# Performance work log

Measured on AMD Instinct MI355X. Metric: run time of the kernel, lower is better.

## Reference

```python
import jax, jax.numpy as jnp
import numpy as np

L = 512       # sequence length
N_AA = 21     # amino-acid alphabet size
D = 128       # per-residue substitution embedding dim
N1 = 256
N2 = 256


def setup_inputs() -> dict:
    key = jax.random.key(0)
    k1, k2, k3 = jax.random.split(key, 3)
    X1 = jax.random.randint(k1, (N1, L), 0, N_AA)
    X2 = jax.random.randint(k2, (N2, L), 0, N_AA)
    W = jax.random.normal(k3, (L * N_AA, N_AA * D), dtype=jnp.float32) * 0.02
    b = jnp.zeros((N_AA * D,), jnp.float32)
    w_param = jnp.zeros((L * (L - 1) // 2,), jnp.float32)
    a = jnp.ones((1,), jnp.float32)
    return {"X1": X1, "X2": X2, "W": W, "b": b, "w_param": w_param, "a": a}


def _network(X, W, b):
    # one-hot + linear stand-in for self.network; outputs (n, n_aa, d)
    n = X.shape[0]
    oh = jax.nn.one_hot(X, N_AA, dtype=W.dtype).reshape(n, -1)  # (n, L*n_aa)
    return (oh @ W + b).reshape(n, N_AA, -1)


def _wdk(subs, w):
    # torch: (subs[:, graph] * w).sum(2) * subs, summed over dim 1
    # graph[i] = arange(L), so this equals subs @ w^T contracted with subs:
    # out[..] = sum_i sum_j subs[.., i] * w[i, j] * subs[.., j]
    return jnp.einsum('...i,ij,...j->...', subs, w, subs)


def reference(X1, X2, W, b, w_param, a):
    n1, Lx = X1.shape
    n2 = X2.shape[0]

    # symmetric pairwise weight matrix; diagonal stays 0 -> sigmoid(0)=0.5
    i_x, i_y = np.tril_indices(Lx, k=-1)
    wm = jnp.zeros((Lx, Lx), W.dtype).at[i_x, i_y].set(w_param).at[i_y, i_x].set(w_param)
    w = jax.nn.sigmoid(wm)

    # per-sequence substitution matrices S = E E^T, (n, n_aa, n_aa)
    E1 = _network(X1, W, b)
    S1 = jnp.einsum('nad,nbd->nab', E1, E1)
    E2 = _network(X2, W, b)
    S2 = jnp.einsum('nad,nbd->nab', E2, E2)

    r1 = jnp.arange(n1)
    r2 = jnp.arange(n2)

    # self terms: subs[n, l] = S[n, X[n,l], X[n,l]]
    d1 = S1[r1[:, None], X1, X1]                  # (n1, L)
    k1 = _wdk(d1, w)[:, None]                     # (n1, 1)
    d2 = S2[r2[:, None], X2, X2]                  # (n2, L)
    k2 = _wdk(d2, w)[None, :]                     # (1, n2)

    # cross terms: average of the two sequences' S, gathered directly
    # (avoids materializing the (n1*n2, n_aa, n_aa) averaged S tensor)
    g1 = S1[r1[:, None, None], X1[:, None, :], X2[None, :, :]]  # (n1, n2, L)
    g2 = S2[r2[None, :, None], X1[:, None, :], X2[None, :, :]]  # (n1, n2, L)
    subs = 0.5 * (g1 + g2)

    K = _wdk(subs, w)                             # (n1, n2)
    K = K / jnp.sqrt(k1) / jnp.sqrt(k2)
    return (a ** 2) * K
```

## Files before the change

kernel.cpp:

```cpp
#include <hip/hip_runtime.h>
#include <cstdint>
#include <cstddef>

typedef __attribute__((ext_vector_type(8))) __bf16 bf16x8;
typedef __attribute__((ext_vector_type(4))) float f32x4;
typedef __attribute__((ext_vector_type(16))) float f32x16;

__device__ __forceinline__ unsigned short f2b(float x) {
    uint32_t u = __float_as_uint(x);
    u += 0x7FFFu + ((u >> 16) & 1u);
    return (unsigned short)(u >> 16);
}
__device__ __forceinline__ float b2f(unsigned short h) {
    return __uint_as_float(((uint32_t)h) << 16);
}

__device__ __forceinline__ void gl16(const unsigned short* g, unsigned short* l) {
    __builtin_amdgcn_global_load_lds((const __attribute__((address_space(1))) uint32_t*)g,
                                     (__attribute__((address_space(3))) uint32_t*)l, 16, 0, 0);
}

#define L_SEQ 512
#define N_AA 21
#define DDIM 128
#define NCOL 2688
#define NSEQ 512
#define TBSTRIDE 448
#define KTOT 10752
#define ZCH 12
#define KBTOT 672
#define KBCH 56

#define PB_WBZ   14112
#define PB_EINIT 5376
#define PB_REPACK 1024
#define PB_WBUILD 1024
#define PB_ABZ   2688
#define PB_TOTAL (PB_WBZ + PB_EINIT + PB_REPACK + PB_WBUILD + PB_ABZ)

__global__ __launch_bounds__(256) void prep_kernel(const int* X1, const int* X2,
                                                   const float* W, const float* bvec, const float* wp,
                                                   uint8_t* X8,
                                                   float* w32, unsigned short* wswz,
                                                   float* E, unsigned short* Wbz, unsigned short* Abz) {
    int bid = blockIdx.x;
    int t = threadIdx.x;
    if (bid < PB_WBZ) {
        int f = bid * 4 + (t >> 6);
        int lane = t & 63, lr = lane & 31, hf = lane >> 5;
        int cb = f / KBTOT, kb = f - cb * KBTOT;
        const float* src = W + (size_t)(kb * 16 + hf * 8) * NCOL + cb * 32 + lr;
        union { uint4 q; unsigned short s[8]; } o;
#pragma unroll
        for (int j = 0; j < 8; ++j) o.s[j] = f2b(src[(size_t)j * NCOL]);
        *(uint4*)&Wbz[(size_t)f * 512 + lane * 8] = o.q;
        return;
    }
    bid -= PB_WBZ;
    if (bid < PB_EINIT) {
        int e = bid * 256 + t;
        E[e] = bvec[e % NCOL];
        return;
    }
    bid -= PB_EINIT;
    if (bid < PB_REPACK) {
        int e = bid * 256 + t;
        if (e < 131072) X8[e] = (uint8_t)X1[e];
        else            X8[e] = (uint8_t)X2[e - 131072];
        return;
    }
    bid -= PB_REPACK;
    if (bid < PB_WBUILD) {
        int e = bid * 256 + t;
        int p = e >> 9, q = e & 511;
        float x = 0.0f;
        if (p > q)      x = wp[p * (p - 1) / 2 + q];
        else if (p < q) x = wp[q * (q - 1) / 2 + p];
        float s = 1.0f / (1.0f + expf(-x));
        w32[e] = s;
        int nb = p >> 5, lr = p & 31;
        int kb = q >> 4, hf = (q >> 3) & 1, j = q & 7;
        wswz[(size_t)((nb * 32 + kb) * 512) + (hf * 32 + lr) * 8 + j] = f2b(s);
        return;
    }
    bid -= PB_WBUILD;
    {
        int f = bid * 4 + (t >> 6);
        int lane = t & 63, lr = lane & 31, hf = lane >> 5;
        int mb = f / KBTOT, kb = f - mb * KBTOT;
        int m = mb * 32 + lr;
        const int* Xrow = (m < 256) ? (X1 + (size_t)m * L_SEQ) : (X2 + (size_t)(m - 256) * L_SEQ);
        int k0 = kb * 16 + hf * 8;
        union { uint4 q; unsigned short s[8]; } o;
#pragma unroll
        for (int j = 0; j < 8; ++j) {
            int k = k0 + j;
            int l = k / N_AA;
            int aa = k - l * N_AA;
            o.s[j] = (Xrow[l] == aa) ? (unsigned short)0x3F80u : (unsigned short)0u;
        }
        *(uint4*)&Abz[(size_t)f * 512 + lane * 8] = o.q;
    }
}

__global__ __launch_bounds__(256, 4) void e_mfma_v3(const unsigned short* Abz, const unsigned short* Wbz, float* E) {
    __shared__ unsigned short lds[4 * 8 * 512];

    int lin = blockIdx.x;
    int s = ((lin & 7) * 126) + (lin >> 3);
    int cx = s % 21;
    int rem = s / 21;
    int my = rem & 3;
    int kz = rem >> 2;

    int t = threadIdx.x, wid = t >> 6, lane = t & 63;
    int lr = lane & 31, hf = lane >> 5;
    int kb0 = kz * KBCH;

    const unsigned short* Aw = Abz + ((size_t)((my * 4 + wid) * KBTOT + kb0)) * 512 + lane * 8;
    const unsigned short* Bw = Wbz + ((size_t)((cx * 4 + wid) * KBTOT + kb0)) * 512 + lane * 8;
    unsigned short* La = &lds[wid * 512];
    unsigned short* Lb = &lds[(4 + wid) * 512];

#define STG(buf_, kb_) do { \
        gl16(Aw + (size_t)(kb_) * 512, La + (buf_) * 4096); \
        gl16(Bw + (size_t)(kb_) * 512, Lb + (buf_) * 4096); \
    } while (0)

    int alo = (wid & 1) * 2;
    int blo = 4 + (wid >> 1) * 2;

    f32x16 acc00, acc01, acc10, acc11;
#pragma unroll
    for (int r = 0; r < 16; ++r) { acc00[r] = 0.f; acc01[r] = 0.f; acc10[r] = 0.f; acc11[r] = 0.f; }

#define COMPUTE(kb_) do { \
        const unsigned short* base = &lds[((kb_) & 3) * 4096]; \
        bf16x8 a0 = *(const bf16x8*)(base + (alo + 0) * 512 + lane * 8); \
        bf16x8 a1 = *(const bf16x8*)(base + (alo + 1) * 512 + lane * 8); \
        bf16x8 b0 = *(const bf16x8*)(base + (blo + 0) * 512 + lane * 8); \
        bf16x8 b1 = *(const bf16x8*)(base + (blo + 1) * 512 + lane * 8); \
        acc00 = __builtin_amdgcn_mfma_f32_32x32x16_bf16(a0, b0, acc00, 0, 0, 0); \
        acc01 = __builtin_amdgcn_mfma_f32_32x32x16_bf16(a0, b1, acc01, 0, 0, 0); \
        acc10 = __builtin_amdgcn_mfma_f32_32x32x16_bf16(a1, b0, acc10, 0, 0, 0); \
        acc11 = __builtin_amdgcn_mfma_f32_32x32x16_bf16(a1, b1, acc11, 0, 0, 0); \
    } while (0)

    STG(0, 0); STG(1, 1); STG(2, 2);

#pragma unroll 1
    for (int kb = 0; kb < KBCH - 3; ++kb) {
        STG((kb + 3) & 3, kb + 3);
        asm volatile("s_waitcnt vmcnt(6)" ::: "memory");
        __builtin_amdgcn_s_barrier();
        __builtin_amdgcn_sched_barrier(0);
        COMPUTE(kb);
        __builtin_amdgcn_sched_barrier(0);
        __builtin_amdgcn_s_barrier();
    }
    asm volatile("s_waitcnt vmcnt(4)" ::: "memory");
    __builtin_amdgcn_s_barrier();
    __builtin_amdgcn_sched_barrier(0);
    COMPUTE(53);
    asm volatile("s_waitcnt vmcnt(2)" ::: "memory");
    __builtin_amdgcn_s_barrier();
    __builtin_amdgcn_sched_barrier(0);
    COMPUTE(54);
    asm volatile("s_waitcnt vmcnt(0)" ::: "memory");
    __builtin_amdgcn_s_barrier();
    __builtin_amdgcn_sched_barrier(0);
    COMPUTE(55);

#undef STG
#undef COMPUTE

    int mb0 = my * 4 + (wid & 1) * 2;
    int cb0 = cx * 4 + (wid >> 1) * 2;
#pragma unroll
    for (int r = 0; r < 16; ++r) {
        int row = (r & 3) + 8 * (r >> 2) + 4 * hf;
        float* base = E + (size_t)(mb0 * 32 + row) * NCOL + cb0 * 32 + lr;
        atomicAdd(base, acc00[r]);
        atomicAdd(base + 32, acc01[r]);
        atomicAdd(base + (size_t)32 * NCOL, acc10[r]);
        atomicAdd(base + (size_t)32 * NCOL + 32, acc11[r]);
    }
}

__global__ __launch_bounds__(256) void t_kernel(const float* E, unsigned short* Tb, float* Tdiag) {
    __shared__ float4 Es4[21 * 33];
    int t = threadIdx.x, n = blockIdx.x;
    for (int e = t; e < 21 * 32; e += 256) {
        int r = e >> 5, d = e & 31;
        Es4[r * 33 + d] = *(const float4*)(E + (size_t)n * NCOL + r * 128 + d * 4);
    }
    __syncthreads();
    for (int e = t; e < 441; e += 256) {
        int r = e / 21, c = e - r * 21;
        const float4* ar = &Es4[r * 33];
        const float4* br = &Es4[c * 33];
        float s = 0.f;
#pragma unroll 8
        for (int d = 0; d < 32; ++d) {
            float4 a = ar[d], b = br[d];
            s += a.x * b.x + a.y * b.y + a.z * b.z + a.w * b.w;
        }
        Tb[(size_t)n * TBSTRIDE + e] = f2b(0.5f * s);
        if (r == c) Tdiag[n * 24 + r] = s;
    }
}

__global__ __launch_bounds__(256) void k_kernel(const uint8_t* X8, const float* Tdiag, const float* w32, float* kinv) {
    __shared__ __align__(16) float dvec[4][512];
    __shared__ float Td[4][21];
    __shared__ float red[4][256];
    int t = threadIdx.x, n0 = blockIdx.x * 4;
    if (t < 84) Td[t / 21][t % 21] = Tdiag[(size_t)(n0 + t / 21) * 24 + (t % 21)];
    __syncthreads();
    for (int e = t; e < 2048; e += 256) {
        int nn = e >> 9, l = e & 511;
        dvec[nn][l] = Td[nn][X8[(size_t)(n0 + nn) * 512 + l]];
    }
    __syncthreads();
    float p0 = 0.f, p1 = 0.f, p2 = 0.f, p3 = 0.f;
    for (int p = t; p < 512; p += 256) {
        const float4* wr4 = (const float4*)(w32 + (size_t)p * 512);
        float d0 = 0.f, d1 = 0.f, d2 = 0.f, d3 = 0.f;
        for (int q = 0; q < 128; ++q) {
            float4 wv = wr4[q];
            float4 a = ((const float4*)dvec[0])[q];
            float4 b = ((const float4*)dvec[1])[q];
            float4 c = ((const float4*)dvec[2])[q];
            float4 d = ((const float4*)dvec[3])[q];
            d0 += wv.x * a.x + wv.y * a.y + wv.z * a.z + wv.w * a.w;
            d1 += wv.x * b.x + wv.y * b.y + wv.z * b.z + wv.w * b.w;
            d2 += wv.x * c.x + wv.y * c.y + wv.z * c.z + wv.w * c.w;
            d3 += wv.x * d.x + wv.y * d.y + wv.z * d.z + wv.w * d.w;
        }
        p0 += dvec[0][p] * d0;
        p1 += dvec[1][p] * d1;
        p2 += dvec[2][p] * d2;
        p3 += dvec[3][p] * d3;
    }
    red[0][t] = p0; red[1][t] = p1; red[2][t] = p2; red[3][t] = p3;
    __syncthreads();
    for (int s = 128; s > 0; s >>= 1) {
        if (t < s) {
            red[0][t] += red[0][t + s];
            red[1][t] += red[1][t + s];
            red[2][t] += red[2][t + s];
            red[3][t] += red[3][t + s];
        }
        __syncthreads();
    }
    if (t < 4) kinv[n0 + t] = 1.0f / sqrtf(red[t][0]);
}

__global__ __launch_bounds__(512, 6) void k4_kernel(const uint8_t* X8, const unsigned short* Tb,
                                                    const unsigned short* wswz, const float* kinv,
                                                    const float* Ainp, float* out) {
    __shared__ unsigned short Sh[32 * 520];
    __shared__ unsigned short Ts1h[4 * TBSTRIDE];
    __shared__ unsigned short Ts2h[8 * TBSTRIDE];
    __shared__ unsigned short A21[4 * 512];
    __shared__ uint8_t Xs2[8 * 512];
    __shared__ float Kacc[8][32];

    int t = threadIdx.x;
    int i0 = blockIdx.x * 4;
    int j0 = blockIdx.y * 8;

    for (int e = t; e < 4 * 512; e += 512)
        A21[e] = (unsigned short)(21 * X8[(size_t)(i0 + (e >> 9)) * 512 + (e & 511)]);
    {
        const uint32_t* s2 = (const uint32_t*)(X8 + (size_t)(256 + j0) * 512);
        uint32_t* d2 = (uint32_t*)Xs2;
        for (int e = t; e < 1024; e += 512) d2[e] = s2[e];
    }
    {
        uint32_t* d1 = (uint32_t*)Ts1h;
        for (int e = t; e < 4 * 224; e += 512) {
            int r = e / 224, w = e - r * 224;
            d1[e] = ((const uint32_t*)(Tb + (size_t)(i0 + r) * TBSTRIDE))[w];
        }
        uint32_t* d2 = (uint32_t*)Ts2h;
        for (int e = t; e < 8 * 224; e += 512) {
            int r = e / 224, w = e - r * 224;
            d2[e] = ((const uint32_t*)(Tb + (size_t)(256 + j0 + r) * TBSTRIDE))[w];
        }
    }
    __syncthreads();

    for (int e4 = t; e4 < 32 * 128; e4 += 512) {
        int pr = e4 >> 7, p = (e4 & 127) * 4;
        int ti = pr >> 3, tj = pr & 7;
        uint64_t a4 = *(const uint64_t*)&A21[ti * 512 + p];
        uint32_t b4 = *(const uint32_t*)&Xs2[tj * 512 + p];
        const unsigned short* T1 = &Ts1h[ti * TBSTRIDE];
        const unsigned short* T2 = &Ts2h[tj * TBSTRIDE];
        uint64_t outw = 0;
#pragma unroll
        for (int u = 0; u < 4; ++u) {
            int idx = (int)((a4 >> (16 * u)) & 0xFFFFu) + (int)((b4 >> (8 * u)) & 0xFFu);
            float v = b2f(T1[idx]) + b2f(T2[idx]);
            outw |= (uint64_t)f2b(v) << (16 * u);
        }
        *(uint64_t*)&Sh[pr * 520 + p] = outw;
    }
    __syncthreads();

    int wid = t >> 6, lane = t & 63;
    int lr = lane & 31, hf = lane >> 5;
    int n_base = wid * 64;

    const unsigned short* Sa = &Sh[lr * 520 + hf * 8];
    const unsigned short* Bz0 = wswz + (size_t)((wid * 2 + 0) * 32) * 512 + lane * 8;
    const unsigned short* Bz1 = wswz + (size_t)((wid * 2 + 1) * 32) * 512 + lane * 8;

    f32x16 acc0, acc1;
#pragma unroll
    for (int j = 0; j < 16; ++j) { acc0[j] = 0.f; acc1[j] = 0.f; }

#pragma unroll 2
    for (int kt = 0; kt < 32; ++kt) {
        bf16x8 av = *(const bf16x8*)(Sa + kt * 16);
        bf16x8 bv0 = *(const bf16x8*)(Bz0 + kt * 512);
        bf16x8 bv1 = *(const bf16x8*)(Bz1 + kt * 512);
        acc0 = __builtin_amdgcn_mfma_f32_32x32x16_bf16(av, bv0, acc0, 0, 0, 0);
        acc1 = __builtin_amdgcn_mfma_f32_32x32x16_bf16(av, bv1, acc1, 0, 0, 0);
    }

    float prow[16];
#pragma unroll
    for (int r = 0; r < 16; ++r) {
        int row = (r & 3) + 8 * (r >> 2) + 4 * hf;
        float v = acc0[r] * b2f(Sh[row * 520 + (n_base + lr)]);
        v      += acc1[r] * b2f(Sh[row * 520 + (n_base + 32 + lr)]);
        prow[r] = v;
    }
#pragma unroll
    for (int r = 0; r < 16; ++r) {
        float v = prow[r];
        v += __shfl_xor(v, 1);
        v += __shfl_xor(v, 2);
        v += __shfl_xor(v, 4);
        v += __shfl_xor(v, 8);
        v += __shfl_xor(v, 16);
        if (lr == 0) {
            int row = (r & 3) + 8 * (r >> 2) + 4 * hf;
            Kacc[wid][row] = v;
        }
    }
    __syncthreads();

    if (t < 32) {
        float K = Kacc[0][t] + Kacc[1][t] + Kacc[2][t] + Kacc[3][t]
                + Kacc[4][t] + Kacc[5][t] + Kacc[6][t] + Kacc[7][t];
        int ti = t >> 3, tj = t & 7;
        int i = i0 + ti, j = j0 + tj;
        float a0 = Ainp[0];
        out[i * 256 + j] = a0 * a0 * K * kinv[i] * kinv[256 + j];
    }
}

extern "C" void kernel_launch(void* const* d_in, const int* in_sizes, int n_in,
                              void* d_out, int out_size, void* d_ws, size_t ws_size,
                              hipStream_t stream) {
    const int*   X1 = (const int*)d_in[0];
    const int*   X2 = (const int*)d_in[1];
    const float* W  = (const float*)d_in[2];
    const float* b  = (const float*)d_in[3];
    const float* wp = (const float*)d_in[4];
    const float* a  = (const float*)d_in[5];
    float* out = (float*)d_out;

    char* ws = (char*)d_ws;
    float*          E     = (float*)(ws + 0);
    unsigned short* Tb    = (unsigned short*)(ws + 5505024);
    float*          Tdiag = (float*)(ws + 5963776);
    float*          w32   = (float*)(ws + 6012928);
    unsigned short* wswz  = (unsigned short*)(ws + 7061504);
    float*          kinv  = (float*)(ws + 7585792);
    uint8_t*        X8    = (uint8_t*)(ws + 7587840);
    unsigned short* Abz   = (unsigned short*)(ws + 7849984);
    unsigned short* Wbz   = (unsigned short*)(ws + 18860032);

    prep_kernel<<<PB_TOTAL, 256, 0, stream>>>(X1, X2, W, b, wp, X8, w32, wswz, E, Wbz, Abz);
    e_mfma_v3<<<1008, 256, 0, stream>>>(Abz, Wbz, E);
    t_kernel<<<512, 256, 0, stream>>>(E, Tb, Tdiag);
    k_kernel<<<128, 256, 0, stream>>>(X8, Tdiag, w32, kinv);
    k4_kernel<<<dim3(64, 32), 512, 0, stream>>>(X8, Tb, wswz, kinv, a, out);
}
```

Measured before the change: 376.3 us.

## Replace split-K atomics with per-slab partial stores and restructure k_kernel reduction

New measurement: 327.4 us. 1.15x faster.

```diff
diff --git a/kernel.cpp b/kernel.cpp
--- a/kernel.cpp
+++ b/kernel.cpp
@@ -27,22 +27,21 @@
 #define NSEQ 512
 #define TBSTRIDE 448
 #define KTOT 10752
-#define ZCH 12
+#define ZCH 8
 #define KBTOT 672
-#define KBCH 56
+#define KBCH 84
 
 #define PB_WBZ   14112
-#define PB_EINIT 5376
 #define PB_REPACK 1024
 #define PB_WBUILD 1024
 #define PB_ABZ   2688
-#define PB_TOTAL (PB_WBZ + PB_EINIT + PB_REPACK + PB_WBUILD + PB_ABZ)
+#define PB_TOTAL (PB_WBZ + PB_REPACK + PB_WBUILD + PB_ABZ)
 
 __global__ __launch_bounds__(256) void prep_kernel(const int* X1, const int* X2,
-                                                   const float* W, const float* bvec, const float* wp,
+                                                   const float* W, const float* wp,
                                                    uint8_t* X8,
                                                    float* w32, unsigned short* wswz,
-                                                   float* E, unsigned short* Wbz, unsigned short* Abz) {
+                                                   unsigned short* Wbz, unsigned short* Abz) {
     int bid = blockIdx.x;
     int t = threadIdx.x;
     if (bid < PB_WBZ) {
@@ -57,12 +56,6 @@
         return;
     }
     bid -= PB_WBZ;
-    if (bid < PB_EINIT) {
-        int e = bid * 256 + t;
-        E[e] = bvec[e % NCOL];
-        return;
-    }
-    bid -= PB_EINIT;
     if (bid < PB_REPACK) {
         int e = bid * 256 + t;
         if (e < 131072) X8[e] = (uint8_t)X1[e];
@@ -103,11 +96,11 @@
     }
 }
 
-__global__ __launch_bounds__(256, 4) void e_mfma_v3(const unsigned short* Abz, const unsigned short* Wbz, float* E) {
+__global__ __launch_bounds__(256, 4) void e_mfma_v5(const unsigned short* Abz, const unsigned short* Wbz, float* Ep) {
     __shared__ unsigned short lds[4 * 8 * 512];
 
     int lin = blockIdx.x;
-    int s = ((lin & 7) * 126) + (lin >> 3);
+    int s = ((lin & 7) * 84) + (lin >> 3);
     int cx = s % 21;
     int rem = s / 21;
     int my = rem & 3;
@@ -161,38 +154,47 @@
     asm volatile("s_waitcnt vmcnt(4)" ::: "memory");
     __builtin_amdgcn_s_barrier();
     __builtin_amdgcn_sched_barrier(0);
-    COMPUTE(53);
+    COMPUTE(KBCH - 3);
     asm volatile("s_waitcnt vmcnt(2)" ::: "memory");
     __builtin_amdgcn_s_barrier();
     __builtin_amdgcn_sched_barrier(0);
-    COMPUTE(54);
+    COMPUTE(KBCH - 2);
     asm volatile("s_waitcnt vmcnt(0)" ::: "memory");
     __builtin_amdgcn_s_barrier();
     __builtin_amdgcn_sched_barrier(0);
-    COMPUTE(55);
+    COMPUTE(KBCH - 1);
 
 #undef STG
 #undef COMPUTE
 
     int mb0 = my * 4 + (wid & 1) * 2;
     int cb0 = cx * 4 + (wid >> 1) * 2;
+    float* slab = Ep + (size_t)kz * NSEQ * NCOL;
 #pragma unroll
     for (int r = 0; r < 16; ++r) {
         int row = (r & 3) + 8 * (r >> 2) + 4 * hf;
-        float* base = E + (size_t)(mb0 * 32 + row) * NCOL + cb0 * 32 + lr;
-        atomicAdd(base, acc00[r]);
-        atomicAdd(base + 32, acc01[r]);
-        atomicAdd(base + (size_t)32 * NCOL, acc10[r]);
-        atomicAdd(base + (size_t)32 * NCOL + 32, acc11[r]);
-    }
-}
-
-__global__ __launch_bounds__(256) void t_kernel(const float* E, unsigned short* Tb, float* Tdiag) {
+        float* base = slab + (size_t)(mb0 * 32 + row) * NCOL + cb0 * 32 + lr;
+        base[0] = acc00[r];
+        base[32] = acc01[r];
+        base[(size_t)32 * NCOL] = acc10[r];
+        base[(size_t)32 * NCOL + 32] = acc11[r];
+    }
+}
+
+__global__ __launch_bounds__(256) void t_kernel(const float* Ep, const float* bvec,
+                                                unsigned short* Tb, float* Tdiag) {
     __shared__ float4 Es4[21 * 33];
     int t = threadIdx.x, n = blockIdx.x;
-    for (int e = t; e < 21 * 32; e += 256) {
-        int r = e >> 5, d = e & 31;
-        Es4[r * 33 + d] = *(const float4*)(E + (size_t)n * NCOL + r * 128 + d * 4);
+    for (int idx = t; idx < 672; idx += 256) {
+        const float4* bp = (const float4*)(bvec + idx * 4);
+        float4 acc = *bp;
+#pragma unroll
+        for (int z = 0; z < ZCH; ++z) {
+            float4 v = *(const float4*)(Ep + ((size_t)z * NSEQ + n) * NCOL + idx * 4);
+            acc.x += v.x; acc.y += v.y; acc.z += v.z; acc.w += v.w;
+        }
+        int r = idx >> 5, d = idx & 31;
+        Es4[r * 33 + d] = acc;
     }
     __syncthreads();
     for (int e = t; e < 441; e += 256) {
@@ -210,50 +212,64 @@
     }
 }
 
-__global__ __launch_bounds__(256) void k_kernel(const uint8_t* X8, const float* Tdiag, const float* w32, float* kinv) {
+__global__ __launch_bounds__(512) void k_kernel(const uint8_t* X8, const float* Tdiag, const float* w32, float* kinv) {
     __shared__ __align__(16) float dvec[4][512];
     __shared__ float Td[4][21];
-    __shared__ float red[4][256];
+    __shared__ float wred[4][8];
     int t = threadIdx.x, n0 = blockIdx.x * 4;
     if (t < 84) Td[t / 21][t % 21] = Tdiag[(size_t)(n0 + t / 21) * 24 + (t % 21)];
     __syncthreads();
-    for (int e = t; e < 2048; e += 256) {
+    for (int e = t; e < 2048; e += 512) {
         int nn = e >> 9, l = e & 511;
         dvec[nn][l] = Td[nn][X8[(size_t)(n0 + nn) * 512 + l]];
     }
     __syncthreads();
-    float p0 = 0.f, p1 = 0.f, p2 = 0.f, p3 = 0.f;
-    for (int p = t; p < 512; p += 256) {
-        const float4* wr4 = (const float4*)(w32 + (size_t)p * 512);
-        float d0 = 0.f, d1 = 0.f, d2 = 0.f, d3 = 0.f;
-        for (int q = 0; q < 128; ++q) {
-            float4 wv = wr4[q];
-            float4 a = ((const float4*)dvec[0])[q];
-            float4 b = ((const float4*)dvec[1])[q];
-            float4 c = ((const float4*)dvec[2])[q];
-            float4 d = ((const float4*)dvec[3])[q];
-            d0 += wv.x * a.x + wv.y * a.y + wv.z * a.z + wv.w * a.w;
-            d1 += wv.x * b.x + wv.y * b.y + wv.z * b.z + wv.w * b.w;
-            d2 += wv.x * c.x + wv.y * c.y + wv.z * c.z + wv.w * c.w;
-            d3 += wv.x * d.x + wv.y * d.y + wv.z * d.z + wv.w * d.w;
-        }
-        p0 += dvec[0][p] * d0;
-        p1 += dvec[1][p] * d1;
-        p2 += dvec[2][p] * d2;
-        p3 += dvec[3][p] * d3;
-    }
-    red[0][t] = p0; red[1][t] = p1; red[2][t] = p2; red[3][t] = p3;
-    __syncthreads();
-    for (int s = 128; s > 0; s >>= 1) {
-        if (t < s) {
-            red[0][t] += red[0][t + s];
-            red[1][t] += red[1][t + s];
-            red[2][t] += red[2][t + s];
-            red[3][t] += red[3][t + s];
-        }
-        __syncthreads();
-    }
-    if (t < 4) kinv[n0 + t] = 1.0f / sqrtf(red[t][0]);
+    int wid = t >> 6, lane = t & 63;
+    int q0 = lane * 8;
+
+    float4 dA0 = *(const float4*)&dvec[0][q0], dA1 = *(const float4*)&dvec[0][q0 + 4];
+    float4 dB0 = *(const float4*)&dvec[1][q0], dB1 = *(const float4*)&dvec[1][q0 + 4];
+    float4 dC0 = *(const float4*)&dvec[2][q0], dC1 = *(const float4*)&dvec[2][q0 + 4];
+    float4 dD0 = *(const float4*)&dvec[3][q0], dD1 = *(const float4*)&dvec[3][q0 + 4];
+
+    float4 rA0 = {0,0,0,0}, rA1 = {0,0,0,0}, rB0 = {0,0,0,0}, rB1 = {0,0,0,0};
+    float4 rC0 = {0,0,0,0}, rC1 = {0,0,0,0}, rD0 = {0,0,0,0}, rD1 = {0,0,0,0};
+
+#define FMA4(R, W, S) do { (R).x += (W).x * (S); (R).y += (W).y * (S); (R).z += (W).z * (S); (R).w += (W).w * (S); } while (0)
+    for (int p = wid; p < 512; p += 8) {
+        const float4* wr = (const float4*)(w32 + (size_t)p * 512 + q0);
+        float4 w0v = wr[0], w1v = wr[1];
+        float a = dvec[0][p], b = dvec[1][p], c = dvec[2][p], d = dvec[3][p];
+        FMA4(rA0, w0v, a); FMA4(rA1, w1v, a);
+        FMA4(rB0, w0v, b); FMA4(rB1, w1v, b);
+        FMA4(rC0, w0v, c); FMA4(rC1, w1v, c);
+        FMA4(rD0, w0v, d); FMA4(rD1, w1v, d);
+    }
+#undef FMA4
+
+#define DOT8(R0, R1, D0, D1) ((R0).x*(D0).x + (R0).y*(D0).y + (R0).z*(D0).z + (R0).w*(D0).w + \
+                              (R1).x*(D1).x + (R1).y*(D1).y + (R1).z*(D1).z + (R1).w*(D1).w)
+    float s0 = DOT8(rA0, rA1, dA0, dA1);
+    float s1 = DOT8(rB0, rB1, dB0, dB1);
+    float s2 = DOT8(rC0, rC1, dC0, dC1);
+    float s3 = DOT8(rD0, rD1, dD0, dD1);
+#undef DOT8
+
+#pragma unroll
+    for (int off = 1; off < 64; off <<= 1) {
+        s0 += __shfl_xor(s0, off);
+        s1 += __shfl_xor(s1, off);
+        s2 += __shfl_xor(s2, off);
+        s3 += __shfl_xor(s3, off);
+    }
+    if (lane == 0) { wred[0][wid] = s0; wred[1][wid] = s1; wred[2][wid] = s2; wred[3][wid] = s3; }
+    __syncthreads();
+    if (t < 4) {
+        float kk = 0.f;
+#pragma unroll
+        for (int w = 0; w < 8; ++w) kk += wred[t][w];
+        kinv[n0 + t] = 1.0f / sqrtf(kk);
+    }
 }
 
 __global__ __launch_bounds__(512, 6) void k4_kernel(const uint8_t* X8, const unsigned short* Tb,
@@ -375,19 +391,19 @@
     float* out = (float*)d_out;
 
     char* ws = (char*)d_ws;
-    float*          E     = (float*)(ws + 0);
-    unsigned short* Tb    = (unsigned short*)(ws + 5505024);
-    float*          Tdiag = (float*)(ws + 5963776);
-    float*          w32   = (float*)(ws + 6012928);
-    unsigned short* wswz  = (unsigned short*)(ws + 7061504);
-    float*          kinv  = (float*)(ws + 7585792);
-    uint8_t*        X8    = (uint8_t*)(ws + 7587840);
-    unsigned short* Abz   = (unsigned short*)(ws + 7849984);
-    unsigned short* Wbz   = (unsigned short*)(ws + 18860032);
-
-    prep_kernel<<<PB_TOTAL, 256, 0, stream>>>(X1, X2, W, b, wp, X8, w32, wswz, E, Wbz, Abz);
-    e_mfma_v3<<<1008, 256, 0, stream>>>(Abz, Wbz, E);
-    t_kernel<<<512, 256, 0, stream>>>(E, Tb, Tdiag);
-    k_kernel<<<128, 256, 0, stream>>>(X8, Tdiag, w32, kinv);
+    unsigned short* Tb    = (unsigned short*)(ws + 0);
+    float*          Tdiag = (float*)(ws + 458752);
+    float*          w32   = (float*)(ws + 507904);
+    unsigned short* wswz  = (unsigned short*)(ws + 1556480);
+    float*          kinv  = (float*)(ws + 2080768);
+    uint8_t*        X8    = (uint8_t*)(ws + 2082816);
+    unsigned short* Abz   = (unsigned short*)(ws + 2344960);
+    unsigned short* Wbz   = (unsigned short*)(ws + 13355008);
+    float*          Ep    = (float*)(ws + 71157760);
+
+    prep_kernel<<<PB_TOTAL, 256, 0, stream>>>(X1, X2, W, wp, X8, w32, wswz, Wbz, Abz);
+    e_mfma_v5<<<672, 256, 0, stream>>>(Abz, Wbz, Ep);
+    t_kernel<<<512, 256, 0, stream>>>(Ep, b, Tb, Tdiag);
+    k_kernel<<<128, 512, 0, stream>>>(X8, Tdiag, w32, kinv);
     k4_kernel<<<dim3(64, 32), 512, 0, stream>>>(X8, Tb, wswz, kinv, a, out);
 }
```
